# Optimization experiments

Measured on AMD Instinct MI355X. Metric: run time of the kernel, lower is better.

The kernel has to match this reference:

```python
import jax, jax.numpy as jnp
import numpy as np

NEG_INF = -1e30  # stand-in for float('-inf') that is softmax-safe


def setup_inputs() -> dict:
    key = jax.random.key(0)
    ks = jax.random.split(key, 6)
    B, H, S, D = 2, 8, 1024, 64
    NF, K = 4, 3
    return {
        "query": jax.random.normal(ks[0], (B, H, S, D), dtype=jnp.float32),
        "keys": jax.random.normal(ks[1], (B, H, S, D), dtype=jnp.float32),
        "vals": jax.random.normal(ks[2], (B, H, S, D), dtype=jnp.float32),
        "mask": jnp.ones((B, 1, S, S), dtype=jnp.int32),
        "conv_w": jax.random.normal(ks[3], (NF, 1, K, K), dtype=jnp.float32) * (1.0 / K),
        "conv_b": jnp.zeros((NF,), dtype=jnp.float32),
        "lin_w": jax.random.normal(ks[4], (1, NF), dtype=jnp.float32) * 0.5,
        "lin_b": jnp.zeros((1,), dtype=jnp.float32),
    }


def reference(query, keys, vals, mask, conv_w, conv_b, lin_w, lin_b):
    B, H, S, D = query.shape
    NF = conv_w.shape[0]
    K = conv_w.shape[2]
    scale = jnp.asarray(D, query.dtype) ** 0.5

    # [B,H,S,S] raw dot-product scores
    dp = jnp.einsum("bhsd,bhtd->bhst", query, keys) / scale

    # conv2d over the score matrix: treat (B*H) as batch, 1 input channel
    x = dp.reshape(B * H, 1, S, S)
    conv = jax.lax.conv_general_dilated(
        x, conv_w,
        window_strides=(1, 1),
        padding=[(K // 2, K // 2), (K // 2, K // 2)],
        dimension_numbers=("NCHW", "OIHW", "NCHW"),
    ) + conv_b[None, :, None, None]
    conv = jax.nn.leaky_relu(conv, negative_slope=0.01)  # [B*H, NF, S, S]

    # per-pixel linear over the filter axis (Linear(num_filters, 1))
    conv = conv.reshape(B, H, NF, S, S)
    preattn = jnp.einsum("bhfst,f->bhst", conv, lin_w[0]) + lin_b[0]

    # masking + softmax (mask broadcasts over heads)
    preattn = jnp.where(mask == 0, jnp.asarray(NEG_INF, preattn.dtype), preattn)
    attn = jax.nn.softmax(preattn, axis=-1)

    # dropout is identity in eval mode
    return jnp.einsum("bhst,bhtd->bhsd", attn, vals)
```

## Files before the change

kernel.cpp:

```cpp
#include <hip/hip_runtime.h>
#include <math.h>

#define S_LEN 1024
#define D_DIM 64
#define NBH   16

typedef unsigned short ushort_t;
typedef __attribute__((ext_vector_type(8))) short short8;
typedef __attribute__((ext_vector_type(4))) short short4v;
typedef __attribute__((ext_vector_type(4))) float f32x4;
typedef __attribute__((ext_vector_type(2))) float f32x2;

__device__ __forceinline__ ushort_t rne_bf16(float x) {
    unsigned u = __float_as_uint(x);
    return (ushort_t)((u + 0x7FFFu + ((u >> 16) & 1u)) >> 16);
}
__device__ __forceinline__ void split1(float x, ushort_t& h, ushort_t& l) {
    h = rne_bf16(x);
    float hf = __uint_as_float((unsigned)h << 16);
    l = rne_bf16(x - hf);
}

__global__ __launch_bounds__(256) void prep(
    const float* __restrict__ k, const float* __restrict__ v,
    const int* __restrict__ mask,
    ushort_t* __restrict__ khi, ushort_t* __restrict__ klo,
    ushort_t* __restrict__ vhi, ushort_t* __restrict__ vlo,
    unsigned* __restrict__ mw)
{
    __shared__ float Ls[64][65];
    const int tid = threadIdx.x;
    const int bx = blockIdx.x;
    if (bx < 512) {
        const int gid  = bx * 256 + tid;
        const int bh   = gid >> 13;
        const int tile = (gid >> 7) & 63;
        const int ch   = (gid >> 6) & 1;
        const int lane = gid & 63;
        const int quad = lane >> 4, t15 = lane & 15;
        const float* src = k + ((size_t)bh * S_LEN + tile * 16 + t15) * D_DIM
                             + ch * 32 + quad * 8;
        float x[8];
        *(float4*)(x + 0) = *(const float4*)(src);
        *(float4*)(x + 4) = *(const float4*)(src + 4);
        short8 hv, lv;
        #pragma unroll
        for (int i = 0; i < 8; ++i) {
            ushort_t h, l;
            split1(x[i], h, l);
            hv[i] = (short)h; lv[i] = (short)l;
        }
        *(short8*)(khi + (size_t)gid * 8) = hv;
        *(short8*)(klo + (size_t)gid * 8) = lv;
    } else if (bx < 768) {
        const int bi = bx - 512;
        const int tt = bi & 15, bh = bi >> 4;
        const float* vb = v + ((size_t)bh * S_LEN + tt * 64) * D_DIM;
        #pragma unroll
        for (int p = 0; p < 4; ++p) {
            int idx = p * 1024 + tid * 4;
            int r = idx >> 6, c = idx & 63;
            float4 x = *(const float4*)(vb + r * 64 + c);
            Ls[r][c] = x.x; Ls[r][c+1] = x.y; Ls[r][c+2] = x.z; Ls[r][c+3] = x.w;
        }
        __syncthreads();
        const int d = tid >> 2, c0 = (tid & 3) * 16;
        ushort_t hi[16], lo[16];
        #pragma unroll
        for (int j = 0; j < 16; ++j) split1(Ls[c0 + j][d], hi[j], lo[j]);
        const int tb0 = tt * 8 + (c0 >> 3);
        const size_t o0 = (((size_t)bh * 128 + tb0) * 64 + d) * 8;
        const size_t o1 = (((size_t)bh * 128 + tb0 + 1) * 64 + d) * 8;
        *(short8*)(vhi + o0) = *(short8*)(hi);
        *(short8*)(vhi + o1) = *(short8*)(hi + 8);
        *(short8*)(vlo + o0) = *(short8*)(lo);
        *(short8*)(vlo + o1) = *(short8*)(lo + 8);
    } else {
        const int gid = (bx - 768) * 256 + tid;
        const int row = gid >> 5, wd = gid & 31;
        const int4* mp = (const int4*)(mask + (size_t)row * 1024 + wd * 32);
        unsigned bits = 0;
        #pragma unroll
        for (int p = 0; p < 8; ++p) {
            int4 qv = mp[p];
            bits |= (qv.x != 0 ? 1u : 0u) << (p * 4 + 0);
            bits |= (qv.y != 0 ? 1u : 0u) << (p * 4 + 1);
            bits |= (qv.z != 0 ? 1u : 0u) << (p * 4 + 2);
            bits |= (qv.w != 0 ? 1u : 0u) << (p * 4 + 3);
        }
        mw[(size_t)row * 32 + wd] = bits;
    }
}

__global__ __launch_bounds__(256) void qk_mfma(
    const float* __restrict__ q,
    const ushort_t* __restrict__ khi, const ushort_t* __restrict__ klo,
    float* __restrict__ dp)
{
    __shared__ float Ls[4][16][68];
    const int st = blockIdx.x, bh = blockIdx.y;
    const int s0 = st * 16;
    const int tid = threadIdx.x;
    const int wave = tid >> 6, lane = tid & 63;
    const int m = lane & 15, quad = lane >> 4;

    const float* qp = q + ((size_t)bh * S_LEN + s0 + m) * D_DIM + quad * 8;
    float qa[16];
    *(float4*)(qa + 0)  = *(const float4*)(qp + 0);
    *(float4*)(qa + 4)  = *(const float4*)(qp + 4);
    *(float4*)(qa + 8)  = *(const float4*)(qp + 32);
    *(float4*)(qa + 12) = *(const float4*)(qp + 36);
    short8 ahi0, alo0, ahi1, alo1;
    #pragma unroll
    for (int i = 0; i < 8; ++i) {
        ushort_t h, l;
        split1(qa[i], h, l);      ahi0[i] = (short)h; alo0[i] = (short)l;
        split1(qa[8 + i], h, l);  ahi1[i] = (short)h; alo1[i] = (short)l;
    }

    float* dpb = dp + ((size_t)bh * S_LEN + s0) * S_LEN;

    #pragma unroll
    for (int sub = 0; sub < 4; ++sub) {
        #pragma unroll
        for (int tt = 0; tt < 4; ++tt) {
            const int tile = wave * 16 + sub * 4 + tt;
            const size_t kb = (((size_t)bh * 64 + tile) * 128 + lane) * 8;
            short8 bhi0 = *(const short8*)(khi + kb);
            short8 blo0 = *(const short8*)(klo + kb);
            short8 bhi1 = *(const short8*)(khi + kb + 512);
            short8 blo1 = *(const short8*)(klo + kb + 512);
            f32x4 acc = {0.f, 0.f, 0.f, 0.f};
            acc = __builtin_amdgcn_mfma_f32_16x16x32_bf16(ahi0, bhi0, acc, 0, 0, 0);
            acc = __builtin_amdgcn_mfma_f32_16x16x32_bf16(ahi0, blo0, acc, 0, 0, 0);
            acc = __builtin_amdgcn_mfma_f32_16x16x32_bf16(alo0, bhi0, acc, 0, 0, 0);
            acc = __builtin_amdgcn_mfma_f32_16x16x32_bf16(ahi1, bhi1, acc, 0, 0, 0);
            acc = __builtin_amdgcn_mfma_f32_16x16x32_bf16(ahi1, blo1, acc, 0, 0, 0);
            acc = __builtin_amdgcn_mfma_f32_16x16x32_bf16(alo1, bhi1, acc, 0, 0, 0);
            #pragma unroll
            for (int r = 0; r < 4; ++r)
                Ls[wave][quad * 4 + r][tt * 16 + m] = acc[r] * 0.125f;
        }
        const int cb = wave * 256 + sub * 64;
        #pragma unroll
        for (int p = 0; p < 4; ++p) {
            const int row = p * 4 + (lane >> 4);
            const int f4  = lane & 15;
            float4 val = *(const float4*)&Ls[wave][row][f4 * 4];
            *(float4*)&dpb[(size_t)row * S_LEN + cb + f4 * 4] = val;
        }
    }
}

#define PSTR 1048
__global__ __launch_bounds__(512) void conv_av(
    const float* __restrict__ dp, const unsigned* __restrict__ mw,
    const ushort_t* __restrict__ vhi, const ushort_t* __restrict__ vlo,
    const float* __restrict__ conv_w, const float* __restrict__ conv_b,
    const float* __restrict__ lin_w, const float* __restrict__ lin_b,
    float* __restrict__ out)
{
    __shared__ ushort_t pP[16 * PSTR];
    __shared__ float oBuf[16][68];
    __shared__ float lsPart[16][4];
    __shared__ unsigned mb[16][32];

    const int st = blockIdx.x, bh = blockIdx.y;
    const int s0 = st * 16;
    const int b  = bh >> 3;
    const int tid = threadIdx.x;
    const int wave = tid >> 6, lane = tid & 63;
    const int m = lane & 15, quad = lane >> 4;

    {
        const int row = tid >> 5, wd = tid & 31;
        mb[row][wd] = mw[((size_t)b * S_LEN + s0 + row) * 32 + wd];
    }

    float w[36];
    #pragma unroll
    for (int i = 0; i < 36; ++i) w[i] = conv_w[i];
    float cb[4], lw[4];
    #pragma unroll
    for (int f = 0; f < 4; ++f) { cb[f] = conv_b[f]; lw[f] = lin_w[f]; }
    const float lb = lin_b[0];

    const int rh = tid >> 8, cg = tid & 255, c0 = cg * 4;
    const float* dpb = dp + (size_t)bh * S_LEN * S_LEN;
    __syncthreads();

    #pragma unroll
    for (int pass = 0; pass < 2; ++pass) {
        const int obase = rh * 8 + pass * 4;
        float rowv[6][6];
        #pragma unroll
        for (int jj = 0; jj < 6; ++jj) {
            const int ir = s0 + obase - 1 + jj;
            if (ir >= 0 && ir < S_LEN) {
                const float* rp = dpb + (size_t)ir * S_LEN + c0;
                f32x4 md = *(const f32x4*)rp;
                rowv[jj][0] = cg ? rp[-1] : 0.f;
                rowv[jj][1] = md.x; rowv[jj][2] = md.y;
                rowv[jj][3] = md.z; rowv[jj][4] = md.w;
                rowv[jj][5] = (cg < 255) ? rp[4] : 0.f;
            } else {
                #pragma unroll
                for (int i = 0; i < 6; ++i) rowv[jj][i] = 0.f;
            }
        }
        float ls[4];
        #pragma unroll
        for (int jo = 0; jo < 4; ++jo) {
            const int o = obase + jo;
            f32x2 pa = {lb, lb}, pb = {lb, lb};
            #pragma unroll
            for (int f = 0; f < 4; ++f) {
                f32x2 ca = {cb[f], cb[f]}, cbv = ca;
                #pragma unroll
                for (int dr = 0; dr < 3; ++dr) {
                    const float* vv = rowv[jo + dr];
                    #pragma unroll
                    for (int dc = 0; dc < 3; ++dc) {
                        const float wt = w[f * 9 + dr * 3 + dc];
                        f32x2 ia = {vv[dc],     vv[dc + 1]};
                        f32x2 ib = {vv[dc + 2], vv[dc + 3]};
                        ca  += wt * ia;
                        cbv += wt * ib;
                    }
                }
                f32x2 la  = {fmaxf(ca.x, 0.f)  + 0.01f * fminf(ca.x, 0.f),
                             fmaxf(ca.y, 0.f)  + 0.01f * fminf(ca.y, 0.f)};
                f32x2 lb2 = {fmaxf(cbv.x, 0.f) + 0.01f * fminf(cbv.x, 0.f),
                             fmaxf(cbv.y, 0.f) + 0.01f * fminf(cbv.y, 0.f)};
                pa += lw[f] * la;
                pb += lw[f] * lb2;
            }
            const unsigned word = mb[o][cg >> 3];
            const unsigned nib  = (word >> ((cg & 7) * 4)) & 0xFu;
            float pre[4] = {pa.x, pa.y, pb.x, pb.y};
            #pragma unroll
            for (int i = 0; i < 4; ++i)
                if (!((nib >> i) & 1u)) pre[i] = -1e30f;
            float pv[4];
            #pragma unroll
            for (int i = 0; i < 4; ++i) pv[i] = __expf(pre[i]);
            ls[jo] = (pv[0] + pv[1]) + (pv[2] + pv[3]);
            short4v hv = {(short)rne_bf16(pv[0]), (short)rne_bf16(pv[1]),
                          (short)rne_bf16(pv[2]), (short)rne_bf16(pv[3])};
            *(short4v*)&pP[o * PSTR + c0] = hv;
        }
        #pragma unroll
        for (int jo = 0; jo < 4; ++jo) {
            float t = ls[jo];
            #pragma unroll
            for (int off = 1; off < 64; off <<= 1) t += __shfl_xor(t, off);
            if (lane == 0) lsPart[obase + jo][wave & 3] = t;
        }
    }
    __syncthreads();

    const int d0 = (wave & 3) * 16;
    const int th = wave >> 2;
    f32x4 O = {0.f, 0.f, 0.f, 0.f};
    #pragma unroll 4
    for (int i = 0; i < 16; ++i) {
        const int c = th * 16 + i;
        short8 ph = *(const short8*)&pP[m * PSTR + c * 32 + quad * 8];
        const size_t vb = (((size_t)bh * 128 + c * 4 + quad) * 64 + d0 + m) * 8;
        short8 vh = *(const short8*)(vhi + vb);
        short8 vl = *(const short8*)(vlo + vb);
        O = __builtin_amdgcn_mfma_f32_16x16x32_bf16(ph, vh, O, 0, 0, 0);
        O = __builtin_amdgcn_mfma_f32_16x16x32_bf16(ph, vl, O, 0, 0, 0);
    }
    if (wave < 4) {
        #pragma unroll
        for (int r = 0; r < 4; ++r) oBuf[quad * 4 + r][d0 + m] = O[r];
    }
    __syncthreads();
    if (wave >= 4) {
        #pragma unroll
        for (int r = 0; r < 4; ++r) {
            const int br = quad * 4 + r;
            const float lsum = (lsPart[br][0] + lsPart[br][1]) +
                               (lsPart[br][2] + lsPart[br][3]);
            out[((size_t)bh * S_LEN + s0 + br) * D_DIM + d0 + m] =
                (O[r] + oBuf[br][d0 + m]) / lsum;
        }
    }
}

extern "C" void kernel_launch(void* const* d_in, const int* in_sizes, int n_in,
                              void* d_out, int out_size, void* d_ws, size_t ws_size,
                              hipStream_t stream) {
    const float* q      = (const float*)d_in[0];
    const float* k      = (const float*)d_in[1];
    const float* v      = (const float*)d_in[2];
    const int*   mask   = (const int*)d_in[3];
    const float* conv_w = (const float*)d_in[4];
    const float* conv_b = (const float*)d_in[5];
    const float* lin_w  = (const float*)d_in[6];
    const float* lin_b  = (const float*)d_in[7];
    float* out = (float*)d_out;

    char* wsb = (char*)d_ws;
    const size_t MB = 1024 * 1024;
    ushort_t* khi = (ushort_t*)(wsb + 0 * MB);
    ushort_t* klo = (ushort_t*)(wsb + 2 * MB);
    ushort_t* vhi = (ushort_t*)(wsb + 4 * MB);
    ushort_t* vlo = (ushort_t*)(wsb + 6 * MB);
    unsigned* mw  = (unsigned*)(wsb + 8 * MB);
    float*    dp  = (float*)(wsb + 16 * MB);

    prep<<<dim3(1024), 256, 0, stream>>>(k, v, mask, khi, klo, vhi, vlo, mw);
    qk_mfma<<<dim3(64, NBH), 256, 0, stream>>>(q, khi, klo, dp);
    conv_av<<<dim3(64, NBH), 512, 0, stream>>>(
        dp, mw, vhi, vlo, conv_w, conv_b, lin_w, lin_b, out);
}
```

Baseline: 136.2 us.

## Split QK and conv/AV kernels across column strips with partial-sum finalize

After: 140.7 us. 3.3% more time.

```diff
diff --git a/kernel.cpp b/kernel.cpp
--- a/kernel.cpp
+++ b/kernel.cpp
@@ -98,7 +98,7 @@
     float* __restrict__ dp)
 {
     __shared__ float Ls[4][16][68];
-    const int st = blockIdx.x, bh = blockIdx.y;
+    const int strip = blockIdx.x, st = blockIdx.y, bh = blockIdx.z;
     const int s0 = st * 16;
     const int tid = threadIdx.x;
     const int wave = tid >> 6, lane = tid & 63;
@@ -121,60 +121,59 @@
     float* dpb = dp + ((size_t)bh * S_LEN + s0) * S_LEN;
 
     #pragma unroll
-    for (int sub = 0; sub < 4; ++sub) {
-        #pragma unroll
-        for (int tt = 0; tt < 4; ++tt) {
-            const int tile = wave * 16 + sub * 4 + tt;
-            const size_t kb = (((size_t)bh * 64 + tile) * 128 + lane) * 8;
-            short8 bhi0 = *(const short8*)(khi + kb);
-            short8 blo0 = *(const short8*)(klo + kb);
-            short8 bhi1 = *(const short8*)(khi + kb + 512);
-            short8 blo1 = *(const short8*)(klo + kb + 512);
-            f32x4 acc = {0.f, 0.f, 0.f, 0.f};
-            acc = __builtin_amdgcn_mfma_f32_16x16x32_bf16(ahi0, bhi0, acc, 0, 0, 0);
-            acc = __builtin_amdgcn_mfma_f32_16x16x32_bf16(ahi0, blo0, acc, 0, 0, 0);
-            acc = __builtin_amdgcn_mfma_f32_16x16x32_bf16(alo0, bhi0, acc, 0, 0, 0);
-            acc = __builtin_amdgcn_mfma_f32_16x16x32_bf16(ahi1, bhi1, acc, 0, 0, 0);
-            acc = __builtin_amdgcn_mfma_f32_16x16x32_bf16(ahi1, blo1, acc, 0, 0, 0);
-            acc = __builtin_amdgcn_mfma_f32_16x16x32_bf16(alo1, bhi1, acc, 0, 0, 0);
-            #pragma unroll
-            for (int r = 0; r < 4; ++r)
-                Ls[wave][quad * 4 + r][tt * 16 + m] = acc[r] * 0.125f;
-        }
-        const int cb = wave * 256 + sub * 64;
-        #pragma unroll
-        for (int p = 0; p < 4; ++p) {
-            const int row = p * 4 + (lane >> 4);
-            const int f4  = lane & 15;
-            float4 val = *(const float4*)&Ls[wave][row][f4 * 4];
-            *(float4*)&dpb[(size_t)row * S_LEN + cb + f4 * 4] = val;
-        }
-    }
-}
-
-#define PSTR 1048
-__global__ __launch_bounds__(512) void conv_av(
+    for (int tt = 0; tt < 4; ++tt) {
+        const int tile = strip * 16 + wave * 4 + tt;
+        const size_t kb = (((size_t)bh * 64 + tile) * 128 + lane) * 8;
+        short8 bhi0 = *(const short8*)(khi + kb);
+        short8 blo0 = *(const short8*)(klo + kb);
+        short8 bhi1 = *(const short8*)(khi + kb + 512);
+        short8 blo1 = *(const short8*)(klo + kb + 512);
+        f32x4 acc = {0.f, 0.f, 0.f, 0.f};
+        acc = __builtin_amdgcn_mfma_f32_16x16x32_bf16(ahi0, bhi0, acc, 0, 0, 0);
+        acc = __builtin_amdgcn_mfma_f32_16x16x32_bf16(ahi0, blo0, acc, 0, 0, 0);
+        acc = __builtin_amdgcn_mfma_f32_16x16x32_bf16(alo0, bhi0, acc, 0, 0, 0);
+        acc = __builtin_amdgcn_mfma_f32_16x16x32_bf16(ahi1, bhi1, acc, 0, 0, 0);
+        acc = __builtin_amdgcn_mfma_f32_16x16x32_bf16(ahi1, blo1, acc, 0, 0, 0);
+        acc = __builtin_amdgcn_mfma_f32_16x16x32_bf16(alo1, bhi1, acc, 0, 0, 0);
+        #pragma unroll
+        for (int r = 0; r < 4; ++r)
+            Ls[wave][quad * 4 + r][tt * 16 + m] = acc[r] * 0.125f;
+    }
+    const int cb = strip * 256 + wave * 64;
+    #pragma unroll
+    for (int p = 0; p < 4; ++p) {
+        const int row = p * 4 + (lane >> 4);
+        const int f4  = lane & 15;
+        float4 val = *(const float4*)&Ls[wave][row][f4 * 4];
+        *(float4*)&dpb[(size_t)row * S_LEN + cb + f4 * 4] = val;
+    }
+}
+
+#define PH 520
+__global__ __launch_bounds__(512) void conv_av_half(
     const float* __restrict__ dp, const unsigned* __restrict__ mw,
     const ushort_t* __restrict__ vhi, const ushort_t* __restrict__ vlo,
     const float* __restrict__ conv_w, const float* __restrict__ conv_b,
     const float* __restrict__ lin_w, const float* __restrict__ lin_b,
-    float* __restrict__ out)
+    float* __restrict__ opart, float* __restrict__ lpart)
 {
-    __shared__ ushort_t pP[16 * PSTR];
+    __shared__ ushort_t pP[16 * PH];
     __shared__ float oBuf[16][68];
-    __shared__ float lsPart[16][4];
-    __shared__ unsigned mb[16][32];
-
-    const int st = blockIdx.x, bh = blockIdx.y;
+    __shared__ float lsPart[16][2];
+    __shared__ unsigned mb[16][16];
+
+    const int hx = blockIdx.x, bh = blockIdx.y;
+    const int st = hx >> 1, half = hx & 1;
     const int s0 = st * 16;
+    const int T0 = half * 512;
     const int b  = bh >> 3;
     const int tid = threadIdx.x;
     const int wave = tid >> 6, lane = tid & 63;
     const int m = lane & 15, quad = lane >> 4;
 
-    {
-        const int row = tid >> 5, wd = tid & 31;
-        mb[row][wd] = mw[((size_t)b * S_LEN + s0 + row) * 32 + wd];
+    if (tid < 256) {
+        const int row = tid >> 4, wd = tid & 15;
+        mb[row][wd] = mw[((size_t)b * S_LEN + s0 + row) * 32 + half * 16 + wd];
     }
 
     float w[36];
@@ -185,13 +184,14 @@
     for (int f = 0; f < 4; ++f) { cb[f] = conv_b[f]; lw[f] = lin_w[f]; }
     const float lb = lin_b[0];
 
-    const int rh = tid >> 8, cg = tid & 255, c0 = cg * 4;
+    const int rh = tid >> 7, cg = tid & 127;
+    const int lc0 = cg * 4;
+    const int c0  = T0 + lc0;
     const float* dpb = dp + (size_t)bh * S_LEN * S_LEN;
     __syncthreads();
 
-    #pragma unroll
-    for (int pass = 0; pass < 2; ++pass) {
-        const int obase = rh * 8 + pass * 4;
+    {
+        const int obase = rh * 4;
         float rowv[6][6];
         #pragma unroll
         for (int jj = 0; jj < 6; ++jj) {
@@ -199,10 +199,10 @@
             if (ir >= 0 && ir < S_LEN) {
                 const float* rp = dpb + (size_t)ir * S_LEN + c0;
                 f32x4 md = *(const f32x4*)rp;
-                rowv[jj][0] = cg ? rp[-1] : 0.f;
+                rowv[jj][0] = (c0 > 0)    ? rp[-1] : 0.f;
                 rowv[jj][1] = md.x; rowv[jj][2] = md.y;
                 rowv[jj][3] = md.z; rowv[jj][4] = md.w;
-                rowv[jj][5] = (cg < 255) ? rp[4] : 0.f;
+                rowv[jj][5] = (c0 < 1020) ? rp[4]  : 0.f;
             } else {
                 #pragma unroll
                 for (int i = 0; i < 6; ++i) rowv[jj][i] = 0.f;
@@ -247,26 +247,31 @@
             ls[jo] = (pv[0] + pv[1]) + (pv[2] + pv[3]);
             short4v hv = {(short)rne_bf16(pv[0]), (short)rne_bf16(pv[1]),
                           (short)rne_bf16(pv[2]), (short)rne_bf16(pv[3])};
-            *(short4v*)&pP[o * PSTR + c0] = hv;
-        }
+            *(short4v*)&pP[o * PH + lc0] = hv;
+        }
+        const int wg = (tid >> 6) & 1;
         #pragma unroll
         for (int jo = 0; jo < 4; ++jo) {
             float t = ls[jo];
             #pragma unroll
             for (int off = 1; off < 64; off <<= 1) t += __shfl_xor(t, off);
-            if (lane == 0) lsPart[obase + jo][wave & 3] = t;
+            if (lane == 0) lsPart[obase + jo][wg] = t;
         }
     }
     __syncthreads();
 
+    const size_t tile = (size_t)(st * NBH + bh) * 2 + half;
+    if (tid < 16) lpart[tile * 16 + tid] = lsPart[tid][0] + lsPart[tid][1];
+
     const int d0 = (wave & 3) * 16;
-    const int th = wave >> 2;
+    const int tq = wave >> 2;
     f32x4 O = {0.f, 0.f, 0.f, 0.f};
-    #pragma unroll 4
-    for (int i = 0; i < 16; ++i) {
-        const int c = th * 16 + i;
-        short8 ph = *(const short8*)&pP[m * PSTR + c * 32 + quad * 8];
-        const size_t vb = (((size_t)bh * 128 + c * 4 + quad) * 64 + d0 + m) * 8;
+    #pragma unroll
+    for (int i = 0; i < 8; ++i) {
+        const int cl = tq * 8 + i;
+        const int cgl = half * 16 + cl;
+        short8 ph = *(const short8*)&pP[m * PH + cl * 32 + quad * 8];
+        const size_t vb = (((size_t)bh * 128 + cgl * 4 + quad) * 64 + d0 + m) * 8;
         short8 vh = *(const short8*)(vhi + vb);
         short8 vl = *(const short8*)(vlo + vb);
         O = __builtin_amdgcn_mfma_f32_16x16x32_bf16(ph, vh, O, 0, 0, 0);
@@ -281,12 +286,28 @@
         #pragma unroll
         for (int r = 0; r < 4; ++r) {
             const int br = quad * 4 + r;
-            const float lsum = (lsPart[br][0] + lsPart[br][1]) +
-                               (lsPart[br][2] + lsPart[br][3]);
-            out[((size_t)bh * S_LEN + s0 + br) * D_DIM + d0 + m] =
-                (O[r] + oBuf[br][d0 + m]) / lsum;
-        }
-    }
+            opart[tile * 1024 + (size_t)br * 64 + d0 + m] =
+                O[r] + oBuf[br][d0 + m];
+        }
+    }
+}
+
+__global__ __launch_bounds__(256) void finalize(
+    const float* __restrict__ opart, const float* __restrict__ lpart,
+    float* __restrict__ out)
+{
+    const int st = blockIdx.x, bh = blockIdx.y;
+    const int tid = threadIdx.x;
+    const int row = tid >> 4, dq = tid & 15;
+    const size_t t0 = (size_t)(st * NBH + bh) * 2;
+    const float la = lpart[t0 * 16 + row];
+    const float lbv = lpart[(t0 + 1) * 16 + row];
+    const float inv = 1.0f / (la + lbv);
+    f32x4 a = *(const f32x4*)&opart[t0 * 1024 + (size_t)row * 64 + dq * 4];
+    f32x4 b = *(const f32x4*)&opart[(t0 + 1) * 1024 + (size_t)row * 64 + dq * 4];
+    f32x4 o = {(a.x + b.x) * inv, (a.y + b.y) * inv,
+               (a.z + b.z) * inv, (a.w + b.w) * inv};
+    *(f32x4*)&out[((size_t)bh * S_LEN + st * 16 + row) * D_DIM + dq * 4] = o;
 }
 
 extern "C" void kernel_launch(void* const* d_in, const int* in_sizes, int n_in,
@@ -304,15 +325,18 @@
 
     char* wsb = (char*)d_ws;
     const size_t MB = 1024 * 1024;
-    ushort_t* khi = (ushort_t*)(wsb + 0 * MB);
-    ushort_t* klo = (ushort_t*)(wsb + 2 * MB);
-    ushort_t* vhi = (ushort_t*)(wsb + 4 * MB);
-    ushort_t* vlo = (ushort_t*)(wsb + 6 * MB);
-    unsigned* mw  = (unsigned*)(wsb + 8 * MB);
-    float*    dp  = (float*)(wsb + 16 * MB);
+    ushort_t* khi   = (ushort_t*)(wsb + 0 * MB);
+    ushort_t* klo   = (ushort_t*)(wsb + 2 * MB);
+    ushort_t* vhi   = (ushort_t*)(wsb + 4 * MB);
+    ushort_t* vlo   = (ushort_t*)(wsb + 6 * MB);
+    unsigned* mw    = (unsigned*)(wsb + 8 * MB);
+    float*    lpart = (float*)(wsb + 9 * MB);
+    float*    opart = (float*)(wsb + 10 * MB);
+    float*    dp    = (float*)(wsb + 32 * MB);
 
     prep<<<dim3(1024), 256, 0, stream>>>(k, v, mask, khi, klo, vhi, vlo, mw);
-    qk_mfma<<<dim3(64, NBH), 256, 0, stream>>>(q, khi, klo, dp);
-    conv_av<<<dim3(64, NBH), 512, 0, stream>>>(
-        dp, mw, vhi, vlo, conv_w, conv_b, lin_w, lin_b, out);
-}
+    qk_mfma<<<dim3(4, 64, NBH), 256, 0, stream>>>(q, khi, klo, dp);
+    conv_av_half<<<dim3(128, NBH), 512, 0, stream>>>(
+        dp, mw, vhi, vlo, conv_w, conv_b, lin_w, lin_b, opart, lpart);
+    finalize<<<dim3(64, NBH), 256, 0, stream>>>(opart, lpart, out);
+}
```

## Store score matrix in fp16 and compute 3x3 conv with packed fdot2

Applied to the files above, without the earlier changes.

Measured after the change: 140.7 us. 3.3% more time.

```diff
diff --git a/kernel.cpp b/kernel.cpp
--- a/kernel.cpp
+++ b/kernel.cpp
@@ -6,10 +6,11 @@
 #define NBH   16
 
 typedef unsigned short ushort_t;
+typedef unsigned int uint_t;
 typedef __attribute__((ext_vector_type(8))) short short8;
 typedef __attribute__((ext_vector_type(4))) short short4v;
 typedef __attribute__((ext_vector_type(4))) float f32x4;
-typedef __attribute__((ext_vector_type(2))) float f32x2;
+typedef __attribute__((ext_vector_type(2))) _Float16 h2;
 
 __device__ __forceinline__ ushort_t rne_bf16(float x) {
     unsigned u = __float_as_uint(x);
@@ -20,13 +21,32 @@
     float hf = __uint_as_float((unsigned)h << 16);
     l = rne_bf16(x - hf);
 }
+__device__ __forceinline__ ushort_t f16bits(float x) {
+    _Float16 h = (_Float16)x;
+    ushort_t b;
+    __builtin_memcpy(&b, &h, 2);
+    return b;
+}
+__device__ __forceinline__ h2 as_h2(uint_t u) {
+    h2 r;
+    __builtin_memcpy(&r, &u, 4);
+    return r;
+}
+#if __has_builtin(__builtin_amdgcn_fdot2)
+#define FDOT2(a, b, c) __builtin_amdgcn_fdot2((a), (b), (c), false)
+#else
+__device__ __forceinline__ float fdot2_sw(h2 a, h2 b, float c) {
+    return fmaf((float)a[0], (float)b[0], fmaf((float)a[1], (float)b[1], c));
+}
+#define FDOT2(a, b, c) fdot2_sw((a), (b), (c))
+#endif
 
 __global__ __launch_bounds__(256) void prep(
     const float* __restrict__ k, const float* __restrict__ v,
-    const int* __restrict__ mask,
+    const int* __restrict__ mask, const float* __restrict__ conv_w,
     ushort_t* __restrict__ khi, ushort_t* __restrict__ klo,
     ushort_t* __restrict__ vhi, ushort_t* __restrict__ vlo,
-    unsigned* __restrict__ mw)
+    unsigned* __restrict__ mw, uint_t* __restrict__ wpk)
 {
     __shared__ float Ls[64][65];
     const int tid = threadIdx.x;
@@ -75,7 +95,7 @@
         *(short8*)(vhi + o1) = *(short8*)(hi + 8);
         *(short8*)(vlo + o0) = *(short8*)(lo);
         *(short8*)(vlo + o1) = *(short8*)(lo + 8);
-    } else {
+    } else if (bx < 1024) {
         const int gid = (bx - 768) * 256 + tid;
         const int row = gid >> 5, wd = gid & 31;
         const int4* mp = (const int4*)(mask + (size_t)row * 1024 + wd * 32);
@@ -89,13 +109,25 @@
             bits |= (qv.w != 0 ? 1u : 0u) << (p * 4 + 3);
         }
         mw[(size_t)row * 32 + wd] = bits;
+    } else {
+        if (tid < 12) {
+            const int f = tid / 3, r = tid % 3;
+            const float w0 = conv_w[f * 9 + r * 3 + 0];
+            const float w1 = conv_w[f * 9 + r * 3 + 1];
+            const float w2 = conv_w[f * 9 + r * 3 + 2];
+            const uint_t b0 = f16bits(w0), b1 = f16bits(w1), b2 = f16bits(w2);
+            const int base = tid * 3;
+            wpk[base + 0] = b0 | (b1 << 16);
+            wpk[base + 1] = b2;
+            wpk[base + 2] = b2 << 16;
+        }
     }
 }
 
 __global__ __launch_bounds__(256) void qk_mfma(
     const float* __restrict__ q,
     const ushort_t* __restrict__ khi, const ushort_t* __restrict__ klo,
-    float* __restrict__ dp)
+    ushort_t* __restrict__ dph)
 {
     __shared__ float Ls[4][16][68];
     const int st = blockIdx.x, bh = blockIdx.y;
@@ -114,11 +146,11 @@
     #pragma unroll
     for (int i = 0; i < 8; ++i) {
         ushort_t h, l;
-        split1(qa[i], h, l);      ahi0[i] = (short)h; alo0[i] = (short)l;
-        split1(qa[8 + i], h, l);  ahi1[i] = (short)h; alo1[i] = (short)l;
-    }
-
-    float* dpb = dp + ((size_t)bh * S_LEN + s0) * S_LEN;
+        split1(qa[i] * 0.125f, h, l);      ahi0[i] = (short)h; alo0[i] = (short)l;
+        split1(qa[8 + i] * 0.125f, h, l);  ahi1[i] = (short)h; alo1[i] = (short)l;
+    }
+
+    ushort_t* dpb = dph + ((size_t)bh * S_LEN + s0) * S_LEN;
 
     #pragma unroll
     for (int sub = 0; sub < 4; ++sub) {
@@ -130,16 +162,16 @@
             short8 blo0 = *(const short8*)(klo + kb);
             short8 bhi1 = *(const short8*)(khi + kb + 512);
             short8 blo1 = *(const short8*)(klo + kb + 512);
-            f32x4 acc = {0.f, 0.f, 0.f, 0.f};
-            acc = __builtin_amdgcn_mfma_f32_16x16x32_bf16(ahi0, bhi0, acc, 0, 0, 0);
-            acc = __builtin_amdgcn_mfma_f32_16x16x32_bf16(ahi0, blo0, acc, 0, 0, 0);
-            acc = __builtin_amdgcn_mfma_f32_16x16x32_bf16(alo0, bhi0, acc, 0, 0, 0);
-            acc = __builtin_amdgcn_mfma_f32_16x16x32_bf16(ahi1, bhi1, acc, 0, 0, 0);
-            acc = __builtin_amdgcn_mfma_f32_16x16x32_bf16(ahi1, blo1, acc, 0, 0, 0);
-            acc = __builtin_amdgcn_mfma_f32_16x16x32_bf16(alo1, bhi1, acc, 0, 0, 0);
+            f32x4 a0 = {0.f, 0.f, 0.f, 0.f}, a1 = {0.f, 0.f, 0.f, 0.f};
+            a0 = __builtin_amdgcn_mfma_f32_16x16x32_bf16(ahi0, bhi0, a0, 0, 0, 0);
+            a1 = __builtin_amdgcn_mfma_f32_16x16x32_bf16(ahi1, bhi1, a1, 0, 0, 0);
+            a0 = __builtin_amdgcn_mfma_f32_16x16x32_bf16(ahi0, blo0, a0, 0, 0, 0);
+            a1 = __builtin_amdgcn_mfma_f32_16x16x32_bf16(ahi1, blo1, a1, 0, 0, 0);
+            a0 = __builtin_amdgcn_mfma_f32_16x16x32_bf16(alo0, bhi0, a0, 0, 0, 0);
+            a1 = __builtin_amdgcn_mfma_f32_16x16x32_bf16(alo1, bhi1, a1, 0, 0, 0);
             #pragma unroll
             for (int r = 0; r < 4; ++r)
-                Ls[wave][quad * 4 + r][tt * 16 + m] = acc[r] * 0.125f;
+                Ls[wave][quad * 4 + r][tt * 16 + m] = a0[r] + a1[r];
         }
         const int cb = wave * 256 + sub * 64;
         #pragma unroll
@@ -147,16 +179,19 @@
             const int row = p * 4 + (lane >> 4);
             const int f4  = lane & 15;
             float4 val = *(const float4*)&Ls[wave][row][f4 * 4];
-            *(float4*)&dpb[(size_t)row * S_LEN + cb + f4 * 4] = val;
+            short4v hv = {(short)f16bits(val.x), (short)f16bits(val.y),
+                          (short)f16bits(val.z), (short)f16bits(val.w)};
+            *(short4v*)&dpb[(size_t)row * S_LEN + cb + f4 * 4] = hv;
         }
     }
 }
 
 #define PSTR 1048
 __global__ __launch_bounds__(512) void conv_av(
-    const float* __restrict__ dp, const unsigned* __restrict__ mw,
+    const ushort_t* __restrict__ dph, const unsigned* __restrict__ mw,
+    const uint_t* __restrict__ wpk,
     const ushort_t* __restrict__ vhi, const ushort_t* __restrict__ vlo,
-    const float* __restrict__ conv_w, const float* __restrict__ conv_b,
+    const float* __restrict__ conv_b,
     const float* __restrict__ lin_w, const float* __restrict__ lin_b,
     float* __restrict__ out)
 {
@@ -177,67 +212,69 @@
         mb[row][wd] = mw[((size_t)b * S_LEN + s0 + row) * 32 + wd];
     }
 
-    float w[36];
-    #pragma unroll
-    for (int i = 0; i < 36; ++i) w[i] = conv_w[i];
     float cb[4], lw[4];
     #pragma unroll
     for (int f = 0; f < 4; ++f) { cb[f] = conv_b[f]; lw[f] = lin_w[f]; }
     const float lb = lin_b[0];
 
     const int rh = tid >> 8, cg = tid & 255, c0 = cg * 4;
-    const float* dpb = dp + (size_t)bh * S_LEN * S_LEN;
+    const ushort_t* dpb = dph + (size_t)bh * S_LEN * S_LEN;
     __syncthreads();
 
     #pragma unroll
     for (int pass = 0; pass < 2; ++pass) {
         const int obase = rh * 8 + pass * 4;
-        float rowv[6][6];
+        uint_t rowp[6][5];
         #pragma unroll
         for (int jj = 0; jj < 6; ++jj) {
             const int ir = s0 + obase - 1 + jj;
             if (ir >= 0 && ir < S_LEN) {
-                const float* rp = dpb + (size_t)ir * S_LEN + c0;
-                f32x4 md = *(const f32x4*)rp;
-                rowv[jj][0] = cg ? rp[-1] : 0.f;
-                rowv[jj][1] = md.x; rowv[jj][2] = md.y;
-                rowv[jj][3] = md.z; rowv[jj][4] = md.w;
-                rowv[jj][5] = (cg < 255) ? rp[4] : 0.f;
+                const ushort_t* rp = dpb + (size_t)ir * S_LEN + c0;
+                uint2 dd = *(const uint2*)rp;
+                uint_t sm1 = cg        ? (uint_t)rp[-1] : 0u;
+                uint_t s4  = (cg < 255) ? (uint_t)rp[4] : 0u;
+                rowp[jj][0] = __builtin_amdgcn_perm(dd.x, sm1, 0x05040100);
+                rowp[jj][1] = dd.x;
+                rowp[jj][2] = __builtin_amdgcn_alignbit(dd.y, dd.x, 16);
+                rowp[jj][3] = dd.y;
+                rowp[jj][4] = __builtin_amdgcn_perm(s4, dd.y, 0x05040302);
             } else {
                 #pragma unroll
-                for (int i = 0; i < 6; ++i) rowv[jj][i] = 0.f;
+                for (int i = 0; i < 5; ++i) rowp[jj][i] = 0u;
             }
         }
         float ls[4];
         #pragma unroll
         for (int jo = 0; jo < 4; ++jo) {
             const int o = obase + jo;
-            f32x2 pa = {lb, lb}, pb = {lb, lb};
+            float pre[4] = {lb, lb, lb, lb};
             #pragma unroll
             for (int f = 0; f < 4; ++f) {
-                f32x2 ca = {cb[f], cb[f]}, cbv = ca;
+                float cv0 = cb[f], cv1 = cv0, cv2 = cv0, cv3 = cv0;
                 #pragma unroll
-                for (int dr = 0; dr < 3; ++dr) {
-                    const float* vv = rowv[jo + dr];
-                    #pragma unroll
-                    for (int dc = 0; dc < 3; ++dc) {
-                        const float wt = w[f * 9 + dr * 3 + dc];
-                        f32x2 ia = {vv[dc],     vv[dc + 1]};
-                        f32x2 ib = {vv[dc + 2], vv[dc + 3]};
-                        ca  += wt * ia;
-                        cbv += wt * ib;
-                    }
+                for (int r = 0; r < 3; ++r) {
+                    const int base = (f * 3 + r) * 3;
+                    const h2 w01 = as_h2(wpk[base + 0]);
+                    const h2 w20 = as_h2(wpk[base + 1]);
+                    const h2 w02 = as_h2(wpk[base + 2]);
+                    const uint_t* P = rowp[jo + r];
+                    cv0 = FDOT2(w01, as_h2(P[0]), cv0);
+                    cv0 = FDOT2(w20, as_h2(P[2]), cv0);
+                    cv1 = FDOT2(w01, as_h2(P[1]), cv1);
+                    cv1 = FDOT2(w20, as_h2(P[3]), cv1);
+                    cv2 = FDOT2(w01, as_h2(P[2]), cv2);
+                    cv2 = FDOT2(w20, as_h2(P[4]), cv2);
+                    cv3 = FDOT2(w01, as_h2(P[3]), cv3);
+                    cv3 = FDOT2(w02, as_h2(P[4]), cv3);
                 }
-                f32x2 la  = {fmaxf(ca.x, 0.f)  + 0.01f * fminf(ca.x, 0.f),
-                             fmaxf(ca.y, 0.f)  + 0.01f * fminf(ca.y, 0.f)};
-                f32x2 lb2 = {fmaxf(cbv.x, 0.f) + 0.01f * fminf(cbv.x, 0.f),
-                             fmaxf(cbv.y, 0.f) + 0.01f * fminf(cbv.y, 0.f)};
-                pa += lw[f] * la;
-                pb += lw[f] * lb2;
+                const float lwf = lw[f];
+                pre[0] = fmaf(lwf, fmaxf(cv0, 0.f) + 0.01f * fminf(cv0, 0.f), pre[0]);
+                pre[1] = fmaf(lwf, fmaxf(cv1, 0.f) + 0.01f * fminf(cv1, 0.f), pre[1]);
+                pre[2] = fmaf(lwf, fmaxf(cv2, 0.f) + 0.01f * fminf(cv2, 0.f), pre[2]);
+                pre[3] = fmaf(lwf, fmaxf(cv3, 0.f) + 0.01f * fminf(cv3, 0.f), pre[3]);
             }
             const unsigned word = mb[o][cg >> 3];
             const unsigned nib  = (word >> ((cg & 7) * 4)) & 0xFu;
-            float pre[4] = {pa.x, pa.y, pb.x, pb.y};
             #pragma unroll
             for (int i = 0; i < 4; ++i)
                 if (!((nib >> i) & 1u)) pre[i] = -1e30f;
@@ -309,10 +346,12 @@
     ushort_t* vhi = (ushort_t*)(wsb + 4 * MB);
     ushort_t* vlo = (ushort_t*)(wsb + 6 * MB);
     unsigned* mw  = (unsigned*)(wsb + 8 * MB);
-    float*    dp  = (float*)(wsb + 16 * MB);
-
-    prep<<<dim3(1024), 256, 0, stream>>>(k, v, mask, khi, klo, vhi, vlo, mw);
-    qk_mfma<<<dim3(64, NBH), 256, 0, stream>>>(q, khi, klo, dp);
+    uint_t*   wpk = (uint_t*)(wsb + 9 * MB);
+    ushort_t* dph = (ushort_t*)(wsb + 16 * MB);
+
+    prep<<<dim3(1025), 256, 0, stream>>>(k, v, mask, conv_w,
+                                         khi, klo, vhi, vlo, mw, wpk);
+    qk_mfma<<<dim3(64, NBH), 256, 0, stream>>>(q, khi, klo, dph);
     conv_av<<<dim3(64, NBH), 512, 0, stream>>>(
-        dp, mw, vhi, vlo, conv_w, conv_b, lin_w, lin_b, out);
-}
+        dph, mw, wpk, vhi, vlo, conv_b, lin_w, lin_b, out);
+}
```

## Retile QK kernel so each wave reuses K fragments across four query row-sets

Applied to the files above, without the earlier changes.

Result: no change. 135.2 us (-0.7%).

```diff
diff --git a/kernel.cpp b/kernel.cpp
--- a/kernel.cpp
+++ b/kernel.cpp
@@ -97,57 +97,73 @@
     const ushort_t* __restrict__ khi, const ushort_t* __restrict__ klo,
     float* __restrict__ dp)
 {
+    __shared__ ushort_t aBuf[4][4][64 * 8];
     __shared__ float Ls[4][16][68];
-    const int st = blockIdx.x, bh = blockIdx.y;
-    const int s0 = st * 16;
+    const int strip = blockIdx.x, sb = blockIdx.y, bh = blockIdx.z;
+    const int s0 = sb * 64;
     const int tid = threadIdx.x;
     const int wave = tid >> 6, lane = tid & 63;
     const int m = lane & 15, quad = lane >> 4;
 
-    const float* qp = q + ((size_t)bh * S_LEN + s0 + m) * D_DIM + quad * 8;
-    float qa[16];
-    *(float4*)(qa + 0)  = *(const float4*)(qp + 0);
-    *(float4*)(qa + 4)  = *(const float4*)(qp + 4);
-    *(float4*)(qa + 8)  = *(const float4*)(qp + 32);
-    *(float4*)(qa + 12) = *(const float4*)(qp + 36);
-    short8 ahi0, alo0, ahi1, alo1;
-    #pragma unroll
-    for (int i = 0; i < 8; ++i) {
-        ushort_t h, l;
-        split1(qa[i], h, l);      ahi0[i] = (short)h; alo0[i] = (short)l;
-        split1(qa[8 + i], h, l);  ahi1[i] = (short)h; alo1[i] = (short)l;
-    }
-
-    float* dpb = dp + ((size_t)bh * S_LEN + s0) * S_LEN;
-
-    #pragma unroll
-    for (int sub = 0; sub < 4; ++sub) {
+    {
+        const float* qp = q + ((size_t)bh * S_LEN + s0 + wave * 16 + m) * D_DIM + quad * 8;
+        float qa[16];
+        *(float4*)(qa + 0)  = *(const float4*)(qp + 0);
+        *(float4*)(qa + 4)  = *(const float4*)(qp + 4);
+        *(float4*)(qa + 8)  = *(const float4*)(qp + 32);
+        *(float4*)(qa + 12) = *(const float4*)(qp + 36);
+        short8 h0, l0, h1, l1;
+        #pragma unroll
+        for (int i = 0; i < 8; ++i) {
+            ushort_t h, l;
+            split1(qa[i] * 0.125f, h, l);      h0[i] = (short)h; l0[i] = (short)l;
+            split1(qa[8 + i] * 0.125f, h, l);  h1[i] = (short)h; l1[i] = (short)l;
+        }
+        *(short8*)&aBuf[wave][0][lane * 8] = h0;
+        *(short8*)&aBuf[wave][1][lane * 8] = h1;
+        *(short8*)&aBuf[wave][2][lane * 8] = l0;
+        *(short8*)&aBuf[wave][3][lane * 8] = l1;
+    }
+    __syncthreads();
+
+    short8 KH0[4], KH1[4], KL0[4], KL1[4];
+    #pragma unroll
+    for (int tt = 0; tt < 4; ++tt) {
+        const int tile = strip * 16 + wave * 4 + tt;
+        const size_t kb = (((size_t)bh * 64 + tile) * 128 + lane) * 8;
+        KH0[tt] = *(const short8*)(khi + kb);
+        KH1[tt] = *(const short8*)(khi + kb + 512);
+        KL0[tt] = *(const short8*)(klo + kb);
+        KL1[tt] = *(const short8*)(klo + kb + 512);
+    }
+
+    const int cb = strip * 256 + wave * 64;
+    #pragma unroll
+    for (int set = 0; set < 4; ++set) {
+        short8 ahi0 = *(const short8*)&aBuf[set][0][lane * 8];
+        short8 ahi1 = *(const short8*)&aBuf[set][1][lane * 8];
+        short8 alo0 = *(const short8*)&aBuf[set][2][lane * 8];
+        short8 alo1 = *(const short8*)&aBuf[set][3][lane * 8];
         #pragma unroll
         for (int tt = 0; tt < 4; ++tt) {
-            const int tile = wave * 16 + sub * 4 + tt;
-            const size_t kb = (((size_t)bh * 64 + tile) * 128 + lane) * 8;
-            short8 bhi0 = *(const short8*)(khi + kb);
-            short8 blo0 = *(const short8*)(klo + kb);
-            short8 bhi1 = *(const short8*)(khi + kb + 512);
-            short8 blo1 = *(const short8*)(klo + kb + 512);
-            f32x4 acc = {0.f, 0.f, 0.f, 0.f};
-            acc = __builtin_amdgcn_mfma_f32_16x16x32_bf16(ahi0, bhi0, acc, 0, 0, 0);
-            acc = __builtin_amdgcn_mfma_f32_16x16x32_bf16(ahi0, blo0, acc, 0, 0, 0);
-            acc = __builtin_amdgcn_mfma_f32_16x16x32_bf16(alo0, bhi0, acc, 0, 0, 0);
-            acc = __builtin_amdgcn_mfma_f32_16x16x32_bf16(ahi1, bhi1, acc, 0, 0, 0);
-            acc = __builtin_amdgcn_mfma_f32_16x16x32_bf16(ahi1, blo1, acc, 0, 0, 0);
-            acc = __builtin_amdgcn_mfma_f32_16x16x32_bf16(alo1, bhi1, acc, 0, 0, 0);
+            f32x4 a0 = {0.f, 0.f, 0.f, 0.f}, a1 = {0.f, 0.f, 0.f, 0.f};
+            a0 = __builtin_amdgcn_mfma_f32_16x16x32_bf16(ahi0, KH0[tt], a0, 0, 0, 0);
+            a1 = __builtin_amdgcn_mfma_f32_16x16x32_bf16(ahi1, KH1[tt], a1, 0, 0, 0);
+            a0 = __builtin_amdgcn_mfma_f32_16x16x32_bf16(ahi0, KL0[tt], a0, 0, 0, 0);
+            a1 = __builtin_amdgcn_mfma_f32_16x16x32_bf16(ahi1, KL1[tt], a1, 0, 0, 0);
+            a0 = __builtin_amdgcn_mfma_f32_16x16x32_bf16(alo0, KH0[tt], a0, 0, 0, 0);
+            a1 = __builtin_amdgcn_mfma_f32_16x16x32_bf16(alo1, KH1[tt], a1, 0, 0, 0);
             #pragma unroll
             for (int r = 0; r < 4; ++r)
-                Ls[wave][quad * 4 + r][tt * 16 + m] = acc[r] * 0.125f;
-        }
-        const int cb = wave * 256 + sub * 64;
+                Ls[wave][quad * 4 + r][tt * 16 + m] = a0[r] + a1[r];
+        }
+        float* rowbase = dp + ((size_t)bh * S_LEN + s0 + set * 16) * S_LEN;
         #pragma unroll
         for (int p = 0; p < 4; ++p) {
             const int row = p * 4 + (lane >> 4);
             const int f4  = lane & 15;
             float4 val = *(const float4*)&Ls[wave][row][f4 * 4];
-            *(float4*)&dpb[(size_t)row * S_LEN + cb + f4 * 4] = val;
+            *(float4*)&rowbase[(size_t)row * S_LEN + cb + f4 * 4] = val;
         }
     }
 }
@@ -312,7 +328,7 @@
     float*    dp  = (float*)(wsb + 16 * MB);
 
     prep<<<dim3(1024), 256, 0, stream>>>(k, v, mask, khi, klo, vhi, vlo, mw);
-    qk_mfma<<<dim3(64, NBH), 256, 0, stream>>>(q, khi, klo, dp);
+    qk_mfma<<<dim3(4, 16, NBH), 256, 0, stream>>>(q, khi, klo, dp);
     conv_av<<<dim3(64, NBH), 512, 0, stream>>>(
         dp, mw, vhi, vlo, conv_w, conv_b, lin_w, lin_b, out);
 }
```
